# Optimization experiments

Measured on AMD Instinct MI355X. Metric: run time of the kernel, lower is better.

## Reference

```python
import jax, jax.numpy as jnp
import numpy as np

H, W = 512, 512
G = 8192
ALPHA_THRESH = 1.0 / 255.0        # meta_f32[0]
TRANS_THRESH = 1.0e-4             # meta_f32[1]
ALPHA_CAP = 0.99                  # meta_f32[6]
BG = jnp.zeros((3,), dtype=jnp.float32)  # config.background


def setup_inputs() -> dict:
    key = jax.random.key(0)
    ks = jax.random.split(key, 7)
    mx = jax.random.uniform(ks[0], (G,), minval=0.0, maxval=float(W))
    my = jax.random.uniform(ks[1], (G,), minval=0.0, maxval=float(H))
    means2d = jnp.stack([mx, my], axis=-1)
    # Build valid conics (inverse 2x2 covariances) from random rotation + scales
    theta = jax.random.uniform(ks[2], (G,), minval=0.0, maxval=2.0 * np.pi)
    s = jax.random.uniform(ks[3], (G, 2), minval=2.0, maxval=12.0)  # px stddevs
    ct, st = jnp.cos(theta), jnp.sin(theta)
    v1, v2 = s[:, 0] ** 2, s[:, 1] ** 2
    ca = ct * ct * v1 + st * st * v2
    cb = ct * st * (v1 - v2)
    cc = st * st * v1 + ct * ct * v2
    det = ca * cc - cb * cb
    conics = jnp.stack([cc / det, -cb / det, ca / det], axis=-1)  # [G,3] = (a,b,c)
    colors = jax.random.uniform(ks[4], (G, 3))
    opacities = jax.random.uniform(ks[5], (G,))
    depths = jax.random.uniform(ks[6], (G,), minval=0.1, maxval=100.0)
    return {"means2d": means2d, "conics": conics, "colors": colors,
            "opacities": opacities, "depths": depths}


def reference(means2d, conics, colors, opacities, depths):
    # Stable front-to-back depth sort (mirrors perm = argsort(depths, stable))
    perm = jnp.argsort(depths, stable=True)
    m = means2d[perm]
    cn = conics[perm]
    col = colors[perm]
    op = opacities[perm]
    a, b, c = cn[:, 0], cn[:, 1], cn[:, 2]
    px = jnp.arange(W, dtype=means2d.dtype) + 0.5  # pixel centers

    def row(y):
        py = y.astype(means2d.dtype) + 0.5
        dx = px[:, None] - m[None, :, 0]          # [W,G]
        dy = py - m[:, 1]                          # [G]
        sigma = 0.5 * (a * dx * dx + c * dy * dy) + b * dx * dy  # [W,G]
        alpha = jnp.minimum(ALPHA_CAP, op * jnp.exp(-sigma))
        alpha = jnp.where((sigma < 0) | (alpha < ALPHA_THRESH), 0.0, alpha)
        # exclusive cumulative transmittance along depth order
        Tprev = jnp.cumprod(1.0 - alpha, axis=-1)
        Tprev = jnp.concatenate([jnp.ones((W, 1), alpha.dtype), Tprev[:, :-1]], axis=-1)
        # early-termination: splats seen after T drops below threshold contribute 0
        wgt = alpha * Tprev * (Tprev >= TRANS_THRESH)  # [W,G]
        rgb = wgt @ col                                 # [W,3]
        t_rem = 1.0 - wgt.sum(axis=-1)                  # remaining transmittance
        return rgb + t_rem[:, None] * BG

    return jax.lax.map(row, jnp.arange(H))  # [H,W,3]
```

## Files before the change

kernel.cpp:

```cpp
#include <hip/hip_runtime.h>

#define G 8192
#define IMG_W 512
#define IMG_H 512
#define TILE 16
#define NTX (IMG_W / TILE)
#define NTY (IMG_H / TILE)
#define BLK 256
#define CAP 1024
#define ALPHA_THRESH (1.0f/255.0f)
#define ALPHA_CAP 0.99f
#define TRANS_THRESH 1e-4f

__global__ __launch_bounds__(BLK)
void range_kernel(const float* __restrict__ means2d,
                  const float* __restrict__ conics,
                  const float* __restrict__ colors,
                  const float* __restrict__ opac,
                  unsigned int* __restrict__ ranges,
                  float* __restrict__ tbl)
{
    int g = blockIdx.x * BLK + threadIdx.x;
    if (g >= G) return;
    float op = opac[g];
    float a  = conics[3*g], b = conics[3*g+1], c = conics[3*g+2];
    float mx = means2d[2*g], my = means2d[2*g+1];
    float cr = colors[3*g], cg = colors[3*g+1], cb = colors[3*g+2];

    float4* t4 = (float4*)(tbl + (g << 4));
    t4[0] = make_float4(mx, my, 0.5f * a, b);
    t4[1] = make_float4(0.5f * c, op, cr, cg);
    t4[2] = make_float4(cb, 0.0f, 0.0f, 0.0f);
    if (g == 0) {
        float4* z = (float4*)(tbl + (G << 4));
        z[0] = z[1] = z[2] = make_float4(0.0f, 0.0f, 0.0f, 0.0f);
    }

    unsigned int packed = 0xFFu;
    if (op * 255.0f >= 1.0f) {
        float smax = __logf(op * 255.0f);
        float det = fmaxf(a * c - b * b, 1e-12f);
        float rx = sqrtf(fmaxf(2.0f * smax * c / det, 0.0f)) * 1.0001f + 0.01f;
        float ry = sqrtf(fmaxf(2.0f * smax * a / det, 0.0f)) * 1.0001f + 0.01f;
        int txmin = (int)ceilf ((mx - rx - 15.5f) * 0.0625f);
        int txmax = (int)floorf((mx + rx -  0.5f) * 0.0625f);
        int tymin = (int)ceilf ((my - ry - 15.5f) * 0.0625f);
        int tymax = (int)floorf((my + ry -  0.5f) * 0.0625f);
        if (!(txmax < 0 || txmin > NTX-1 || tymax < 0 || tymin > NTY-1 ||
              txmin > txmax || tymin > tymax)) {
            txmin = max(txmin, 0); txmax = min(txmax, NTX-1);
            tymin = max(tymin, 0); tymax = min(tymax, NTY-1);
            packed = (unsigned)txmin | ((unsigned)txmax << 8)
                   | ((unsigned)tymin << 16) | ((unsigned)tymax << 24);
        }
    }
    ranges[g] = packed;
}

__device__ __forceinline__ int hitp(unsigned p, unsigned btx, unsigned bty)
{
    return (btx >= (p & 0xffu)) & (btx <= ((p >> 8) & 0xffu)) &
           (bty >= ((p >> 16) & 0xffu)) & (bty <= (p >> 24));
}

__global__ __launch_bounds__(BLK)
void tile_kernel(const unsigned int* __restrict__ ranges,
                 const float* __restrict__ depths,
                 const float* __restrict__ tbl,
                 float*       __restrict__ out)
{
    __shared__ unsigned short slist[CAP + 4];
    __shared__ __align__(16) unsigned int fkeys[CAP + 4];
    __shared__ int woff[4];

    const int tx = threadIdx.x, ty = threadIdx.y;
    const int t = ty * TILE + tx;
    const int lane = t & 63, w = t >> 6;
    const unsigned btx = blockIdx.x, bty = blockIdx.y;

    const uint4* r4 = (const uint4*)ranges;
    const int wbase = w * (G / 4);
    uint4 rv[8];
    #pragma unroll
    for (int i = 0; i < 8; ++i)
        rv[i] = r4[(wbase >> 2) + i * 64 + lane];

    int cnt = 0;
    #pragma unroll
    for (int i = 0; i < 8; ++i)
        cnt += hitp(rv[i].x, btx, bty) + hitp(rv[i].y, btx, bty)
             + hitp(rv[i].z, btx, bty) + hitp(rv[i].w, btx, bty);
    #pragma unroll
    for (int d = 1; d < 64; d <<= 1) cnt += __shfl_xor(cnt, d);
    if (lane == 0) woff[w] = cnt;
    __syncthreads();

    int offs = 0;
    for (int ww = 0; ww < w; ++ww) offs += woff[ww];
    const int N = min(woff[0] + woff[1] + woff[2] + woff[3], CAP);

    const unsigned long long lt = (1ull << lane) - 1ull;
    #pragma unroll
    for (int i = 0; i < 8; ++i) {
        int gbase = wbase + i * 256 + lane * 4;
        int h0 = hitp(rv[i].x, btx, bty), h1 = hitp(rv[i].y, btx, bty);
        int h2 = hitp(rv[i].z, btx, bty), h3 = hitp(rv[i].w, btx, bty);
        unsigned long long m0 = __ballot(h0), m1 = __ballot(h1);
        unsigned long long m2 = __ballot(h2), m3 = __ballot(h3);
        int pos = offs + __popcll(m0 & lt) + __popcll(m1 & lt)
                       + __popcll(m2 & lt) + __popcll(m3 & lt);
        if (h0) { if (pos < CAP) slist[pos] = (unsigned short)(gbase    ); pos++; }
        if (h1) { if (pos < CAP) slist[pos] = (unsigned short)(gbase + 1); pos++; }
        if (h2) { if (pos < CAP) slist[pos] = (unsigned short)(gbase + 2); pos++; }
        if (h3) { if (pos < CAP) slist[pos] = (unsigned short)(gbase + 3); pos++; }
        offs += __popcll(m0) + __popcll(m1) + __popcll(m2) + __popcll(m3);
    }
    __syncthreads();

    unsigned short myidx[4]; unsigned int mykey[4]; int myr[4];
    #pragma unroll
    for (int m = 0; m < 4; ++m) {
        int i = t + m * BLK;
        if (i < N) {
            unsigned idx = slist[i];
            unsigned k = __float_as_uint(depths[idx]);
            myidx[m] = (unsigned short)idx; mykey[m] = k; fkeys[i] = k;
        }
    }
    if (t < 4) fkeys[N + t] = 0xFFFFFFFFu;
    __syncthreads();

    const uint4* fk4 = (const uint4*)fkeys;
    const int nj4 = (N + 3) >> 2;
    #pragma unroll
    for (int m = 0; m < 4; ++m) {
        int i = t + m * BLK;
        if (i < N) {
            unsigned ke = mykey[m]; int r = 0;
            for (int j4 = 0; j4 < nj4; ++j4) {
                uint4 kv = fk4[j4]; int j = j4 << 2;
                r += (int)((kv.x < ke) | ((kv.x == ke) & (j     < i)));
                r += (int)((kv.y < ke) | ((kv.y == ke) & (j + 1 < i)));
                r += (int)((kv.z < ke) | ((kv.z == ke) & (j + 2 < i)));
                r += (int)((kv.w < ke) | ((kv.w == ke) & (j + 3 < i)));
            }
            myr[m] = r;
        }
    }
    __syncthreads();
    #pragma unroll
    for (int m = 0; m < 4; ++m) {
        int i = t + m * BLK;
        if (i < N) slist[myr[m]] = myidx[m];
    }
    if (t < 4) slist[N + t] = (unsigned short)G;
    __syncthreads();

    const float px = (float)(btx * TILE + tx) + 0.5f;
    const float py = (float)(bty * TILE + ty) + 0.5f;
    float T = 1.0f, accr = 0.0f, accg = 0.0f, accb = 0.0f;

    for (int base = 0; base < N; base += 4) {
        ushort4 s4 = *(const ushort4*)&slist[base];
        unsigned short sv[4] = { s4.x, s4.y, s4.z, s4.w };
        #pragma unroll
        for (int u = 0; u < 4; ++u) {
            int idx = __builtin_amdgcn_readfirstlane((int)sv[u]);
            const float* r = tbl + (idx << 4);
            float dx = px - r[0], dy = py - r[1];
            float sig = fmaf(r[2], dx*dx, fmaf(r[4], dy*dy, r[3] * (dx*dy)));
            float al = r[5] * __expf(-sig);
            bool ok = (sig >= 0.0f) && (al >= ALPHA_THRESH);
            al = ok ? fminf(al, ALPHA_CAP) : 0.0f;
            float wgt = al * T;
            accr = fmaf(wgt, r[6], accr);
            accg = fmaf(wgt, r[7], accg);
            accb = fmaf(wgt, r[8], accb);
            T *= (1.0f - al);
        }
        if (__all(T < TRANS_THRESH)) break;
    }

    const int o = (((int)bty * TILE + ty) * IMG_W + (int)btx * TILE + tx) * 3;
    out[o]     = accr;
    out[o + 1] = accg;
    out[o + 2] = accb;
}

extern "C" void kernel_launch(void* const* d_in, const int* in_sizes, int n_in,
                              void* d_out, int out_size, void* d_ws, size_t ws_size,
                              hipStream_t stream)
{
    const float* means2d = (const float*)d_in[0];
    const float* conics  = (const float*)d_in[1];
    const float* colors  = (const float*)d_in[2];
    const float* opac    = (const float*)d_in[3];
    const float* depths  = (const float*)d_in[4];
    float* out = (float*)d_out;
    unsigned int* ranges = (unsigned int*)d_ws;
    float* tbl = (float*)((char*)d_ws + 32 * 1024);

    range_kernel<<<G / BLK, BLK, 0, stream>>>(means2d, conics, colors, opac,
                                              ranges, tbl);
    tile_kernel<<<dim3(NTX, NTY), dim3(TILE, TILE), 0, stream>>>(
        ranges, depths, tbl, out);
}
```

Measured before the change: 94.70 us.

## Process two pixels per thread with 128-thread tile blocks

Halves the tile block to 128 threads, with each thread shading two vertically adjacent pixels. Per-splat table loads and shared dx terms are reused across both pixels, and the binning and rank-sort phases are rescaled to two wavefronts. The cost is more registers per thread and half as many threads for the per-tile binning and sorting work, which now takes more iterations each.

```diff
diff --git a/kernel.cpp b/kernel.cpp
--- a/kernel.cpp
+++ b/kernel.cpp
@@ -7,6 +7,7 @@
 #define NTX (IMG_W / TILE)
 #define NTY (IMG_H / TILE)
 #define BLK 256
+#define BLKT 128
 #define CAP 1024
 #define ALPHA_THRESH (1.0f/255.0f)
 #define ALPHA_CAP 0.99f
@@ -63,31 +64,30 @@
            (bty >= ((p >> 16) & 0xffu)) & (bty <= (p >> 24));
 }
 
-__global__ __launch_bounds__(BLK)
+__global__ __launch_bounds__(BLKT)
 void tile_kernel(const unsigned int* __restrict__ ranges,
                  const float* __restrict__ depths,
                  const float* __restrict__ tbl,
                  float*       __restrict__ out)
 {
-    __shared__ unsigned short slist[CAP + 4];
+    __shared__ __align__(16) unsigned short slist[CAP + 4];
     __shared__ __align__(16) unsigned int fkeys[CAP + 4];
-    __shared__ int woff[4];
-
-    const int tx = threadIdx.x, ty = threadIdx.y;
-    const int t = ty * TILE + tx;
+    __shared__ int woff[2];
+
+    const int t = threadIdx.x;
     const int lane = t & 63, w = t >> 6;
     const unsigned btx = blockIdx.x, bty = blockIdx.y;
 
     const uint4* r4 = (const uint4*)ranges;
-    const int wbase = w * (G / 4);
-    uint4 rv[8];
-    #pragma unroll
-    for (int i = 0; i < 8; ++i)
+    const int wbase = w * (G / 2);
+    uint4 rv[16];
+    #pragma unroll
+    for (int i = 0; i < 16; ++i)
         rv[i] = r4[(wbase >> 2) + i * 64 + lane];
 
     int cnt = 0;
     #pragma unroll
-    for (int i = 0; i < 8; ++i)
+    for (int i = 0; i < 16; ++i)
         cnt += hitp(rv[i].x, btx, bty) + hitp(rv[i].y, btx, bty)
              + hitp(rv[i].z, btx, bty) + hitp(rv[i].w, btx, bty);
     #pragma unroll
@@ -95,13 +95,12 @@
     if (lane == 0) woff[w] = cnt;
     __syncthreads();
 
-    int offs = 0;
-    for (int ww = 0; ww < w; ++ww) offs += woff[ww];
-    const int N = min(woff[0] + woff[1] + woff[2] + woff[3], CAP);
+    int offs = (w == 1) ? woff[0] : 0;
+    const int N = min(woff[0] + woff[1], CAP);
 
     const unsigned long long lt = (1ull << lane) - 1ull;
     #pragma unroll
-    for (int i = 0; i < 8; ++i) {
+    for (int i = 0; i < 16; ++i) {
         int gbase = wbase + i * 256 + lane * 4;
         int h0 = hitp(rv[i].x, btx, bty), h1 = hitp(rv[i].y, btx, bty);
         int h2 = hitp(rv[i].z, btx, bty), h3 = hitp(rv[i].w, btx, bty);
@@ -117,10 +116,10 @@
     }
     __syncthreads();
 
-    unsigned short myidx[4]; unsigned int mykey[4]; int myr[4];
-    #pragma unroll
-    for (int m = 0; m < 4; ++m) {
-        int i = t + m * BLK;
+    unsigned short myidx[8]; unsigned int mykey[8]; int myr[8];
+    #pragma unroll
+    for (int m = 0; m < 8; ++m) {
+        int i = t + m * BLKT;
         if (i < N) {
             unsigned idx = slist[i];
             unsigned k = __float_as_uint(depths[idx]);
@@ -133,8 +132,8 @@
     const uint4* fk4 = (const uint4*)fkeys;
     const int nj4 = (N + 3) >> 2;
     #pragma unroll
-    for (int m = 0; m < 4; ++m) {
-        int i = t + m * BLK;
+    for (int m = 0; m < 8; ++m) {
+        int i = t + m * BLKT;
         if (i < N) {
             unsigned ke = mykey[m]; int r = 0;
             for (int j4 = 0; j4 < nj4; ++j4) {
@@ -149,16 +148,21 @@
     }
     __syncthreads();
     #pragma unroll
-    for (int m = 0; m < 4; ++m) {
-        int i = t + m * BLK;
+    for (int m = 0; m < 8; ++m) {
+        int i = t + m * BLKT;
         if (i < N) slist[myr[m]] = myidx[m];
     }
     if (t < 4) slist[N + t] = (unsigned short)G;
     __syncthreads();
 
-    const float px = (float)(btx * TILE + tx) + 0.5f;
-    const float py = (float)(bty * TILE + ty) + 0.5f;
-    float T = 1.0f, accr = 0.0f, accg = 0.0f, accb = 0.0f;
+    const float px  = (float)(btx * TILE + (lane & 15)) + 0.5f;
+    const int   ry  = lane >> 4;
+    const float py0 = (float)(bty * TILE + w * 8 + ry * 2) + 0.5f;
+    const float py1 = py0 + 1.0f;
+
+    float T0 = 1.0f, T1 = 1.0f;
+    float ar0 = 0.f, ag0 = 0.f, ab0 = 0.f;
+    float ar1 = 0.f, ag1 = 0.f, ab1 = 0.f;
 
     for (int base = 0; base < N; base += 4) {
         ushort4 s4 = *(const ushort4*)&slist[base];
@@ -167,24 +171,35 @@
         for (int u = 0; u < 4; ++u) {
             int idx = __builtin_amdgcn_readfirstlane((int)sv[u]);
             const float* r = tbl + (idx << 4);
-            float dx = px - r[0], dy = py - r[1];
-            float sig = fmaf(r[2], dx*dx, fmaf(r[4], dy*dy, r[3] * (dx*dy)));
-            float al = r[5] * __expf(-sig);
-            bool ok = (sig >= 0.0f) && (al >= ALPHA_THRESH);
-            al = ok ? fminf(al, ALPHA_CAP) : 0.0f;
-            float wgt = al * T;
-            accr = fmaf(wgt, r[6], accr);
-            accg = fmaf(wgt, r[7], accg);
-            accb = fmaf(wgt, r[8], accb);
-            T *= (1.0f - al);
-        }
-        if (__all(T < TRANS_THRESH)) break;
-    }
-
-    const int o = (((int)bty * TILE + ty) * IMG_W + (int)btx * TILE + tx) * 3;
-    out[o]     = accr;
-    out[o + 1] = accg;
-    out[o + 2] = accb;
+            float dx = px - r[0];
+            float dy0 = py0 - r[1], dy1 = py1 - r[1];
+            float sg0 = fmaf(r[2], dx*dx, fmaf(r[4], dy0*dy0, r[3] * (dx*dy0)));
+            float sg1 = fmaf(r[2], dx*dx, fmaf(r[4], dy1*dy1, r[3] * (dx*dy1)));
+            float al0 = r[5] * __expf(-sg0);
+            float al1 = r[5] * __expf(-sg1);
+            bool ok0 = (sg0 >= 0.0f) && (al0 >= ALPHA_THRESH);
+            bool ok1 = (sg1 >= 0.0f) && (al1 >= ALPHA_THRESH);
+            al0 = ok0 ? fminf(al0, ALPHA_CAP) : 0.0f;
+            al1 = ok1 ? fminf(al1, ALPHA_CAP) : 0.0f;
+            float w0 = al0 * T0, w1 = al1 * T1;
+            ar0 = fmaf(w0, r[6], ar0);  ar1 = fmaf(w1, r[6], ar1);
+            ag0 = fmaf(w0, r[7], ag0);  ag1 = fmaf(w1, r[7], ag1);
+            ab0 = fmaf(w0, r[8], ab0);  ab1 = fmaf(w1, r[8], ab1);
+            T0 *= (1.0f - al0);
+            T1 *= (1.0f - al1);
+        }
+        if (__all((T0 < TRANS_THRESH) & (T1 < TRANS_THRESH))) break;
+    }
+
+    const int ox = (int)btx * TILE + (lane & 15);
+    const int oy = (int)bty * TILE + w * 8 + ry * 2;
+    const int o = (oy * IMG_W + ox) * 3;
+    out[o]     = ar0;
+    out[o + 1] = ag0;
+    out[o + 2] = ab0;
+    out[o + 3*IMG_W]     = ar1;
+    out[o + 3*IMG_W + 1] = ag1;
+    out[o + 3*IMG_W + 2] = ab1;
 }
 
 extern "C" void kernel_launch(void* const* d_in, const int* in_sizes, int n_in,
@@ -202,6 +217,6 @@
 
     range_kernel<<<G / BLK, BLK, 0, stream>>>(means2d, conics, colors, opac,
                                               ranges, tbl);
-    tile_kernel<<<dim3(NTX, NTY), dim3(TILE, TILE), 0, stream>>>(
+    tile_kernel<<<dim3(NTX, NTY), dim3(BLKT), 0, stream>>>(
         ranges, depths, tbl, out);
 }
```

Measured after the change: 98.48 us. 4.0% more time.

## Split tile blending into depth-chunked partial composites with a merge pass

Applied to the files above, without the earlier changes.

Separates the fused tile kernel into a sort kernel that writes per-tile sorted lists to global memory and a chunk kernel. The chunk kernel splits each tile's list into four depth chunks, each handled by a 64-thread block whose threads compute four pixels and read splat parameters staged in shared memory. A merge kernel then composites the four partial (rgb, T) results front to back. This exposes more parallelism and replaces per-splat global loads with shared-memory reuse. In exchange it adds two kernel launches, extra global traffic for lists and partials, and loses early termination across chunks.

```diff
diff --git a/kernel.cpp b/kernel.cpp
--- a/kernel.cpp
+++ b/kernel.cpp
@@ -6,11 +6,19 @@
 #define TILE 16
 #define NTX (IMG_W / TILE)
 #define NTY (IMG_H / TILE)
+#define NTILES (NTX * NTY)
 #define BLK 256
+#define BLKB 64
+#define NCHUNK 4
 #define CAP 1024
 #define ALPHA_THRESH (1.0f/255.0f)
 #define ALPHA_CAP 0.99f
 #define TRANS_THRESH 1e-4f
+
+#define OFF_TBL   32768
+#define OFF_LIST  (OFF_TBL + G*64)
+#define OFF_N     (OFF_LIST + NTILES*CAP*2)
+#define OFF_PART  (OFF_N + NTILES*4)
 
 __global__ __launch_bounds__(BLK)
 void range_kernel(const float* __restrict__ means2d,
@@ -31,10 +39,6 @@
     t4[0] = make_float4(mx, my, 0.5f * a, b);
     t4[1] = make_float4(0.5f * c, op, cr, cg);
     t4[2] = make_float4(cb, 0.0f, 0.0f, 0.0f);
-    if (g == 0) {
-        float4* z = (float4*)(tbl + (G << 4));
-        z[0] = z[1] = z[2] = make_float4(0.0f, 0.0f, 0.0f, 0.0f);
-    }
 
     unsigned int packed = 0xFFu;
     if (op * 255.0f >= 1.0f) {
@@ -64,19 +68,19 @@
 }
 
 __global__ __launch_bounds__(BLK)
-void tile_kernel(const unsigned int* __restrict__ ranges,
+void sort_kernel(const unsigned int* __restrict__ ranges,
                  const float* __restrict__ depths,
-                 const float* __restrict__ tbl,
-                 float*       __restrict__ out)
-{
-    __shared__ unsigned short slist[CAP + 4];
-    __shared__ __align__(16) unsigned int fkeys[CAP + 4];
+                 unsigned short* __restrict__ lists,
+                 int* __restrict__ tile_n)
+{
+    __shared__ __align__(16) unsigned short slist[CAP];
+    __shared__ __align__(16) unsigned int fkeys[CAP + 8];
     __shared__ int woff[4];
 
-    const int tx = threadIdx.x, ty = threadIdx.y;
-    const int t = ty * TILE + tx;
+    const int t = threadIdx.x;
     const int lane = t & 63, w = t >> 6;
     const unsigned btx = blockIdx.x, bty = blockIdx.y;
+    const int tile = (int)bty * NTX + (int)btx;
 
     const uint4* r4 = (const uint4*)ranges;
     const int wbase = w * (G / 4);
@@ -127,7 +131,7 @@
             myidx[m] = (unsigned short)idx; mykey[m] = k; fkeys[i] = k;
         }
     }
-    if (t < 4) fkeys[N + t] = 0xFFFFFFFFu;
+    if (t < 8) fkeys[N + t] = 0xFFFFFFFFu;
     __syncthreads();
 
     const uint4* fk4 = (const uint4*)fkeys;
@@ -153,38 +157,126 @@
         int i = t + m * BLK;
         if (i < N) slist[myr[m]] = myidx[m];
     }
-    if (t < 4) slist[N + t] = (unsigned short)G;
-    __syncthreads();
-
-    const float px = (float)(btx * TILE + tx) + 0.5f;
-    const float py = (float)(bty * TILE + ty) + 0.5f;
-    float T = 1.0f, accr = 0.0f, accg = 0.0f, accb = 0.0f;
-
-    for (int base = 0; base < N; base += 4) {
-        ushort4 s4 = *(const ushort4*)&slist[base];
-        unsigned short sv[4] = { s4.x, s4.y, s4.z, s4.w };
-        #pragma unroll
-        for (int u = 0; u < 4; ++u) {
-            int idx = __builtin_amdgcn_readfirstlane((int)sv[u]);
-            const float* r = tbl + (idx << 4);
-            float dx = px - r[0], dy = py - r[1];
-            float sig = fmaf(r[2], dx*dx, fmaf(r[4], dy*dy, r[3] * (dx*dy)));
-            float al = r[5] * __expf(-sig);
-            bool ok = (sig >= 0.0f) && (al >= ALPHA_THRESH);
-            al = ok ? fminf(al, ALPHA_CAP) : 0.0f;
-            float wgt = al * T;
-            accr = fmaf(wgt, r[6], accr);
-            accg = fmaf(wgt, r[7], accg);
-            accb = fmaf(wgt, r[8], accb);
-            T *= (1.0f - al);
-        }
-        if (__all(T < TRANS_THRESH)) break;
-    }
-
-    const int o = (((int)bty * TILE + ty) * IMG_W + (int)btx * TILE + tx) * 3;
-    out[o]     = accr;
-    out[o + 1] = accg;
-    out[o + 2] = accb;
+    __syncthreads();
+
+    for (int i = t; i < N; i += BLK) lists[tile * CAP + i] = slist[i];
+    if (t == 0) tile_n[tile] = N;
+}
+
+__global__ __launch_bounds__(BLKB)
+void chunk_kernel(const unsigned short* __restrict__ lists,
+                  const int* __restrict__ tile_n,
+                  const float* __restrict__ tbl,
+                  float4* __restrict__ partials)
+{
+    __shared__ float4 sq0[BLKB];
+    __shared__ float4 sq1[BLKB];
+    __shared__ float  sq2[BLKB];
+
+    const int bx = blockIdx.x;
+    const int tile = bx >> 2, chunk = bx & 3;
+    const int l = threadIdx.x;
+    const int n = tile_n[tile];
+    const int csz = (n + NCHUNK - 1) >> 2;
+    const int cs = chunk * csz;
+    const int ce = min(n, cs + csz);
+
+    const int tx = tile & (NTX - 1), ty = tile >> 5;
+    const float px  = (float)(tx * TILE + (l & 15)) + 0.5f;
+    const int   y0  = (l >> 4) << 2;
+    const float py0 = (float)(ty * TILE + y0) + 0.5f;
+    const float py1 = py0 + 1.0f, py2 = py0 + 2.0f, py3 = py0 + 3.0f;
+
+    float T0=1.f,T1=1.f,T2=1.f,T3=1.f;
+    float ar0=0.f,ag0=0.f,ab0=0.f, ar1=0.f,ag1=0.f,ab1=0.f;
+    float ar2=0.f,ag2=0.f,ab2=0.f, ar3=0.f,ag3=0.f,ab3=0.f;
+
+    for (int base = cs; base < ce; base += BLKB) {
+        int k = min(BLKB, ce - base);
+        float4 v0 = make_float4(0.f,0.f,0.f,0.f);
+        float4 v1 = make_float4(0.f,0.f,0.f,0.f);
+        float  v2 = 0.f;
+        if (l < k) {
+            int idx = lists[tile * CAP + base + l];
+            const float4* b = (const float4*)(tbl + (idx << 4));
+            v0 = b[0]; v1 = b[1]; v2 = ((const float*)b)[8];
+        }
+        __syncthreads();
+        sq0[l] = v0; sq1[l] = v1; sq2[l] = v2;
+        __syncthreads();
+
+        int k4 = (k + 3) & ~3;
+        bool fin = false;
+        for (int i = 0; i < k4; i += 4) {
+            #pragma unroll
+            for (int u = 0; u < 4; ++u) {
+                float4 q0 = sq0[i + u];
+                float4 q1 = sq1[i + u];
+                float  bl = sq2[i + u];
+                float dx = px - q0.x;
+                float dxdx = dx * dx;
+                float dy0 = py0 - q0.y, dy1 = py1 - q0.y;
+                float dy2 = py2 - q0.y, dy3 = py3 - q0.y;
+                float sg0 = fmaf(q0.z, dxdx, fmaf(q1.x, dy0*dy0, q0.w*(dx*dy0)));
+                float sg1 = fmaf(q0.z, dxdx, fmaf(q1.x, dy1*dy1, q0.w*(dx*dy1)));
+                float sg2 = fmaf(q0.z, dxdx, fmaf(q1.x, dy2*dy2, q0.w*(dx*dy2)));
+                float sg3 = fmaf(q0.z, dxdx, fmaf(q1.x, dy3*dy3, q0.w*(dx*dy3)));
+                float al0 = q1.y * __expf(-sg0);
+                float al1 = q1.y * __expf(-sg1);
+                float al2 = q1.y * __expf(-sg2);
+                float al3 = q1.y * __expf(-sg3);
+                al0 = ((sg0 >= 0.f) && (al0 >= ALPHA_THRESH)) ? fminf(al0, ALPHA_CAP) : 0.f;
+                al1 = ((sg1 >= 0.f) && (al1 >= ALPHA_THRESH)) ? fminf(al1, ALPHA_CAP) : 0.f;
+                al2 = ((sg2 >= 0.f) && (al2 >= ALPHA_THRESH)) ? fminf(al2, ALPHA_CAP) : 0.f;
+                al3 = ((sg3 >= 0.f) && (al3 >= ALPHA_THRESH)) ? fminf(al3, ALPHA_CAP) : 0.f;
+                float w0 = al0*T0, w1 = al1*T1, w2 = al2*T2, w3 = al3*T3;
+                ar0 = fmaf(w0, q1.z, ar0);  ar1 = fmaf(w1, q1.z, ar1);
+                ar2 = fmaf(w2, q1.z, ar2);  ar3 = fmaf(w3, q1.z, ar3);
+                ag0 = fmaf(w0, q1.w, ag0);  ag1 = fmaf(w1, q1.w, ag1);
+                ag2 = fmaf(w2, q1.w, ag2);  ag3 = fmaf(w3, q1.w, ag3);
+                ab0 = fmaf(w0, bl,   ab0);  ab1 = fmaf(w1, bl,   ab1);
+                ab2 = fmaf(w2, bl,   ab2);  ab3 = fmaf(w3, bl,   ab3);
+                T0 *= (1.f - al0);
+                T1 *= (1.f - al1);
+                T2 *= (1.f - al2);
+                T3 *= (1.f - al3);
+            }
+            if (__all((T0 < TRANS_THRESH) & (T1 < TRANS_THRESH) &
+                      (T2 < TRANS_THRESH) & (T3 < TRANS_THRESH))) {
+                fin = true; break;
+            }
+        }
+        if (fin) break;
+    }
+
+    float4* p = partials + ((long)bx << 8);
+    const int xl = l & 15;
+    p[(y0    ) * 16 + xl] = make_float4(ar0, ag0, ab0, T0);
+    p[(y0 + 1) * 16 + xl] = make_float4(ar1, ag1, ab1, T1);
+    p[(y0 + 2) * 16 + xl] = make_float4(ar2, ag2, ab2, T2);
+    p[(y0 + 3) * 16 + xl] = make_float4(ar3, ag3, ab3, T3);
+}
+
+__global__ __launch_bounds__(BLK)
+void merge_kernel(const float4* __restrict__ partials,
+                  float* __restrict__ out)
+{
+    int px = blockIdx.x * BLK + threadIdx.x;
+    int X = px & (IMG_W - 1), Y = px >> 9;
+    int tile = (Y >> 4) * NTX + (X >> 4);
+    int widx = (Y & 15) * 16 + (X & 15);
+    const float4* base = partials + ((long)tile << 10);
+    float4 p0 = base[widx];
+    float4 p1 = base[256 + widx];
+    float4 p2 = base[512 + widx];
+    float4 p3 = base[768 + widx];
+    float r = p3.x, g = p3.y, b = p3.z;
+    r = fmaf(p2.w, r, p2.x); g = fmaf(p2.w, g, p2.y); b = fmaf(p2.w, b, p2.z);
+    r = fmaf(p1.w, r, p1.x); g = fmaf(p1.w, g, p1.y); b = fmaf(p1.w, b, p1.z);
+    r = fmaf(p0.w, r, p0.x); g = fmaf(p0.w, g, p0.y); b = fmaf(p0.w, b, p0.z);
+    out[px*3]     = r;
+    out[px*3 + 1] = g;
+    out[px*3 + 2] = b;
 }
 
 extern "C" void kernel_launch(void* const* d_in, const int* in_sizes, int n_in,
@@ -197,11 +289,18 @@
     const float* opac    = (const float*)d_in[3];
     const float* depths  = (const float*)d_in[4];
     float* out = (float*)d_out;
-    unsigned int* ranges = (unsigned int*)d_ws;
-    float* tbl = (float*)((char*)d_ws + 32 * 1024);
+
+    unsigned int*   ranges   = (unsigned int*)d_ws;
+    float*          tbl      = (float*)((char*)d_ws + OFF_TBL);
+    unsigned short* lists    = (unsigned short*)((char*)d_ws + OFF_LIST);
+    int*            tile_n   = (int*)((char*)d_ws + OFF_N);
+    float4*         partials = (float4*)((char*)d_ws + OFF_PART);
 
     range_kernel<<<G / BLK, BLK, 0, stream>>>(means2d, conics, colors, opac,
                                               ranges, tbl);
-    tile_kernel<<<dim3(NTX, NTY), dim3(TILE, TILE), 0, stream>>>(
-        ranges, depths, tbl, out);
-}
+    sort_kernel<<<dim3(NTX, NTY), BLK, 0, stream>>>(ranges, depths,
+                                                    lists, tile_n);
+    chunk_kernel<<<NTILES * NCHUNK, BLKB, 0, stream>>>(lists, tile_n,
+                                                       tbl, partials);
+    merge_kernel<<<(IMG_W * IMG_H) / BLK, BLK, 0, stream>>>(partials, out);
+}
```

Result: slower. 102.0 us (+7.7%).
